# Performance work log

Hardware: AMD Instinct MI355X
Metric: run time of the kernel (lower is better)

## Reference

```python
import jax, jax.numpy as jnp
import numpy as np

DIST_THRESHOLD = 3.33  # threshold on SQUARED distances (pytorch3d knn_points.dists are squared)


def setup_inputs() -> dict:
    key = jax.random.key(0)
    k1, k2, k3, k4, k5, k6 = jax.random.split(key, 6)
    B, N, D = 4, 8192, 3
    points_src = jax.random.normal(k1, (B, N, D), dtype=jnp.float32)
    points_dst = jax.random.normal(k2, (B, N, D), dtype=jnp.float32)
    flows_pred = jax.random.normal(k3, (B, N, D), dtype=jnp.float32)
    flows_gt = jax.random.normal(k4, (B, N, D), dtype=jnp.float32)
    masks_src = jax.random.randint(k5, (B, N), 0, 2, dtype=jnp.int32)
    masks_dst = jax.random.randint(k6, (B, N), 0, 2, dtype=jnp.int32)
    return {"points_src": points_src, "points_dst": points_dst,
            "flows_pred": flows_pred, "flows_gt": flows_gt,
            "masks_src": masks_src, "masks_dst": masks_dst}


def _pairwise_sq_dists(a, b):
    # a: [N,3], b: [M,3] -> [N,M] squared euclidean distances via gram trick
    a2 = jnp.sum(a * a, axis=-1)  # [N]
    b2 = jnp.sum(b * b, axis=-1)  # [M]
    d2 = a2[:, None] + b2[None, :] - 2.0 * (a @ b.T)
    return jnp.maximum(d2, 0.0)


def _chamfer_thresholded(pw, pd, ms, md):
    # pw: warped src points [N,3]; pd: dst points [M,3]; ms/md: validity masks (>0)
    valid_s = ms > 0  # [N]
    valid_d = md > 0  # [M]
    d2 = _pairwise_sq_dists(pw, pd)  # [N,M]
    # K=1 NN in each direction; invalid points in the *search* set get +inf
    d_wt = jnp.min(jnp.where(valid_d[None, :], d2, jnp.inf), axis=1)  # [N]
    d_tw = jnp.min(jnp.where(valid_s[:, None], d2, jnp.inf), axis=0)  # [M]
    # thresholded mean over valid query points (mirrors boolean-index + .mean())
    sel_wt = valid_s & (d_wt < DIST_THRESHOLD)
    sel_tw = valid_d & (d_tw < DIST_THRESHOLD)
    mean_wt = jnp.sum(jnp.where(sel_wt, d_wt, 0.0)) / jnp.sum(sel_wt)
    mean_tw = jnp.sum(jnp.where(sel_tw, d_tw, 0.0)) / jnp.sum(sel_tw)
    return mean_wt + mean_tw


def reference(points_src, points_dst, flows_pred, flows_gt, masks_src, masks_dst):
    points_src_warped = points_src + flows_pred  # [B,N,3]
    per_sample = jax.vmap(_chamfer_thresholded)(points_src_warped, points_dst,
                                                masks_src, masks_dst)  # [B]
    return jnp.sum(per_sample)
```

## Files before the change

kernel.cpp:

```cpp
#include <hip/hip_runtime.h>
#include <hip/hip_bf16.h>

#define NPTS 8192
#define NB   4
#define BLK  256
#define NREG 32
#define QPT  4
#define NQC  (NREG / QPT)
#define NSL  16
#define SLICE_MAX 512
#define CAP  NPTS
#define THR  3.33f

#define OFF_PSUM 4096
#define OFF_PCNT 8192
#define OFF_BEST 16384
#define OFF_PTS  (16384 + 8 * CAP * 4)

__device__ __forceinline__ unsigned enc_f(float f) {
    unsigned u = __float_as_uint(f);
    return (u & 0x80000000u) ? ~u : (u | 0x80000000u);
}
__device__ __forceinline__ float dec_f(unsigned u) {
    return (u & 0x80000000u) ? __uint_as_float(u & 0x7FFFFFFFu)
                             : __uint_as_float(~u);
}

__global__ __launch_bounds__(BLK) void compact_kernel(
    const float* __restrict__ Ps, const float* __restrict__ Pd,
    const float* __restrict__ F,  const int* __restrict__ Ms,
    const int* __restrict__ Md,   unsigned* __restrict__ bcnt,
    float4* __restrict__ pts,     unsigned* __restrict__ best)
{
    const int b = blockIdx.z, side = blockIdx.y, r = blockIdx.x;
    const int qi = b * 2 + side;
    const int tid = threadIdx.x;
    const int g = b * NPTS + r * BLK + tid;

    best[(size_t)qi * CAP + r * BLK + tid] = 0u;

    float x, y, z; int v;
    if (side == 0) {
        x = Ps[3 * g + 0] + F[3 * g + 0];
        y = Ps[3 * g + 1] + F[3 * g + 1];
        z = Ps[3 * g + 2] + F[3 * g + 2];
        v = Ms[g];
    } else {
        x = Pd[3 * g + 0]; y = Pd[3 * g + 1]; z = Pd[3 * g + 2];
        v = Md[g];
    }
    const bool valid = v > 0;

    const int lane = tid & 63, w = tid >> 6;
    unsigned long long m = __ballot(valid);
    const int my = __popcll(m & ((1ull << lane) - 1ull));
    __shared__ int wc[4];
    if (lane == 0) wc[w] = __popcll(m);
    __syncthreads();
    int off = 0;
#pragma unroll
    for (int i = 0; i < 4; ++i) if (i < w) off += wc[i];
    if (valid)
        pts[(size_t)qi * CAP + r * BLK + off + my] =
            make_float4(2.f * x, 2.f * y, 2.f * z, -(x * x + y * y + z * z));
    if (tid == 0)
        bcnt[qi * NREG + r] = (unsigned)(wc[0] + wc[1] + wc[2] + wc[3]);
}

__global__ __launch_bounds__(BLK) void knn_kernel(
    const unsigned* __restrict__ bcnt, const float4* __restrict__ pts,
    unsigned* __restrict__ best)
{
    const int b = blockIdx.z, d = blockIdx.y;
    const int qc = blockIdx.x / NSL, sl = blockIdx.x % NSL;
    const int qi = b * 2 + d;
    const int si = b * 2 + (1 - d);
    const int tid = threadIdx.x;

    const int r0 = 2 * sl, r1 = 2 * sl + 1;
    const int c0 = (int)bcnt[si * NREG + r0];
    const int c1 = (int)bcnt[si * NREG + r1];
    const int len = c0 + c1;

    __shared__ float4 sp[SLICE_MAX];
    const float4* __restrict__ s0 = pts + (size_t)si * CAP + r0 * BLK;
    const float4* __restrict__ s1 = pts + (size_t)si * CAP + r1 * BLK;
    if (tid < c0) sp[tid] = s0[tid];
    if (tid < c1) sp[c0 + tid] = s1[tid];
    __syncthreads();

    float qx[QPT], qy[QPT], qz[QPT], bt[QPT];
    bool qv[QPT]; int qr[QPT];
#pragma unroll
    for (int k = 0; k < QPT; ++k) {
        qr[k] = qc * QPT + k;
        qv[k] = tid < (int)bcnt[qi * NREG + qr[k]];
        const float4 p = pts[(size_t)qi * CAP + qr[k] * BLK + tid];
        qx[k] = 0.5f * p.x; qy[k] = 0.5f * p.y; qz[k] = 0.5f * p.z;
        bt[k] = -1e30f;
    }

#pragma unroll 4
    for (int j = 0; j < len; ++j) {
        const float4 s = sp[j];
#pragma unroll
        for (int k = 0; k < QPT; ++k) {
            float t = fmaf(qx[k], s.x, s.w);
            t = fmaf(qy[k], s.y, t);
            t = fmaf(qz[k], s.z, t);
            bt[k] = fmaxf(bt[k], t);
        }
    }

#pragma unroll
    for (int k = 0; k < QPT; ++k)
        if (qv[k])
            atomicMax(&best[(size_t)qi * CAP + qr[k] * BLK + tid], enc_f(bt[k]));
}

__global__ __launch_bounds__(BLK) void finalize_kernel(
    const unsigned* __restrict__ bcnt, const float4* __restrict__ pts,
    const unsigned* __restrict__ best, float* __restrict__ psum,
    float* __restrict__ pcnt)
{
    const int b = blockIdx.z, side = blockIdx.y, r = blockIdx.x;
    const int qi = b * 2 + side;
    const int tid = threadIdx.x;
    float s = 0.f, c = 0.f;
    if (tid < (int)bcnt[qi * NREG + r]) {
        const float4 p = pts[(size_t)qi * CAP + r * BLK + tid];
        const float t = dec_f(best[(size_t)qi * CAP + r * BLK + tid]);
        float dd = fmaxf((-p.w) - t, 0.f);
        if (dd < THR) { s = dd; c = 1.f; }
    }
#pragma unroll
    for (int off = 32; off; off >>= 1) {
        s += __shfl_down(s, off);
        c += __shfl_down(c, off);
    }
    __shared__ float red[8];
    const int w = tid >> 6;
    if ((tid & 63) == 0) { red[w] = s; red[4 + w] = c; }
    __syncthreads();
    if (tid == 0) {
        psum[qi * NREG + r] = red[0] + red[1] + red[2] + red[3];
        pcnt[qi * NREG + r] = red[4] + red[5] + red[6] + red[7];
    }
}

__global__ void reduce_out_kernel(const float* __restrict__ psum,
                                  const float* __restrict__ pcnt,
                                  float* __restrict__ out)
{
    const int tid = threadIdx.x;
    float a = 0.f;
    if (tid < 8) {
        float s = 0.f, c = 0.f;
        for (int r = 0; r < NREG; ++r) {
            s += psum[tid * NREG + r];
            c += pcnt[tid * NREG + r];
        }
        a = s / c;
    }
#pragma unroll
    for (int off = 4; off; off >>= 1) a += __shfl_down(a, off);
    if (tid == 0) out[0] = a;
}

extern "C" void kernel_launch(void* const* d_in, const int* in_sizes, int n_in,
                              void* d_out, int out_size, void* d_ws, size_t ws_size,
                              hipStream_t stream)
{
    const float* Ps = (const float*)d_in[0];
    const float* Pd = (const float*)d_in[1];
    const float* F  = (const float*)d_in[2];
    const int* Ms = (const int*)d_in[4];
    const int* Md = (const int*)d_in[5];
    float* out = (float*)d_out;

    unsigned* bcnt = (unsigned*)d_ws;
    float* psum = (float*)((char*)d_ws + OFF_PSUM);
    float* pcnt = (float*)((char*)d_ws + OFF_PCNT);
    unsigned* best = (unsigned*)((char*)d_ws + OFF_BEST);
    float4* pts = (float4*)((char*)d_ws + OFF_PTS);

    compact_kernel<<<dim3(NREG, 2, NB), BLK, 0, stream>>>(
        Ps, Pd, F, Ms, Md, bcnt, pts, best);

    knn_kernel<<<dim3(NQC * NSL, 2, NB), BLK, 0, stream>>>(bcnt, pts, best);

    finalize_kernel<<<dim3(NREG, 2, NB), BLK, 0, stream>>>(
        bcnt, pts, best, psum, pcnt);

    reduce_out_kernel<<<1, 64, 0, stream>>>(psum, pcnt, out);
}
```

Measured before the change: 35.62 us.

## Densely pack valid points via prefix sums to skip empty query and search slots

Each kernel now builds prefix sums over the per-region valid counts and addresses the compacted points as one contiguous logical array, mapping each id to its region by binary search. Query chunks past the valid count exit early, and the search set is split into equal slices, which doubles the slice count. With roughly half of the points masked out, about half of the query blocks can skip their work and the loads are more evenly balanced. The cost is an extra scan and per-point binary search in shared memory, plus an extra sync.

```diff
diff --git a/kernel.cpp b/kernel.cpp
--- a/kernel.cpp
+++ b/kernel.cpp
@@ -6,9 +6,10 @@
 #define BLK  256
 #define NREG 32
 #define QPT  4
-#define NQC  (NREG / QPT)
-#define NSL  16
-#define SLICE_MAX 512
+#define QPB  (QPT * BLK)
+#define NQC_MAX (NPTS / QPB)
+#define NSL  32
+#define SMAX ((NPTS + NSL - 1) / NSL)
 #define CAP  NPTS
 #define THR  3.33f
 
@@ -24,6 +25,29 @@
 __device__ __forceinline__ float dec_f(unsigned u) {
     return (u & 0x80000000u) ? __uint_as_float(u & 0x7FFFFFFFu)
                              : __uint_as_float(~u);
+}
+
+__device__ __forceinline__ void build_prefix(const unsigned* __restrict__ bcnt,
+                                             int qi, int* P, int tid) {
+    if (tid < 64) {
+        const int lane = tid & 63;
+        int v = (lane < NREG) ? (int)bcnt[qi * NREG + lane] : 0;
+#pragma unroll
+        for (int o = 1; o < NREG; o <<= 1) {
+            int t = __shfl_up(v, o);
+            if (lane >= o) v += t;
+        }
+        if (lane < NREG) P[lane + 1] = v;
+        if (lane == 0) P[0] = 0;
+    }
+}
+
+__device__ __forceinline__ int map_region(const int* P, int id) {
+    int r = 0;
+#pragma unroll
+    for (int s = 16; s; s >>= 1)
+        if (P[r + s] <= id) r += s;
+    return r;
 }
 
 __global__ __launch_bounds__(BLK) void compact_kernel(
@@ -77,25 +101,47 @@
     const int si = b * 2 + (1 - d);
     const int tid = threadIdx.x;
 
-    const int r0 = 2 * sl, r1 = 2 * sl + 1;
-    const int c0 = (int)bcnt[si * NREG + r0];
-    const int c1 = (int)bcnt[si * NREG + r1];
-    const int len = c0 + c1;
-
-    __shared__ float4 sp[SLICE_MAX];
-    const float4* __restrict__ s0 = pts + (size_t)si * CAP + r0 * BLK;
-    const float4* __restrict__ s1 = pts + (size_t)si * CAP + r1 * BLK;
-    if (tid < c0) sp[tid] = s0[tid];
-    if (tid < c1) sp[c0 + tid] = s1[tid];
+    __shared__ int Pq[NREG + 1], Psx[NREG + 1];
+    __shared__ float4 sp[SMAX];
+
+    if (tid < 64) {
+        const int lane = tid & 63;
+        int vq = (lane < NREG) ? (int)bcnt[qi * NREG + lane] : 0;
+        int vs = (lane < NREG) ? (int)bcnt[si * NREG + lane] : 0;
+#pragma unroll
+        for (int o = 1; o < NREG; o <<= 1) {
+            int tq = __shfl_up(vq, o);
+            int ts = __shfl_up(vs, o);
+            if (lane >= o) { vq += tq; vs += ts; }
+        }
+        if (lane < NREG) { Pq[lane + 1] = vq; Psx[lane + 1] = vs; }
+        if (lane == 0) { Pq[0] = 0; Psx[0] = 0; }
+    }
+    __syncthreads();
+
+    const int nq = Pq[NREG], ns = Psx[NREG];
+    if (qc * QPB >= nq) return;
+    const int L = (ns + NSL - 1) / NSL;
+    const int start = sl * L;
+    int len = ns - start; if (len > L) len = L;
+    if (len <= 0) return;
+
+    if (tid < len) {
+        const int id = start + tid;
+        const int r = map_region(Psx, id);
+        sp[tid] = pts[(size_t)si * CAP + r * BLK + (id - Psx[r])];
+    }
     __syncthreads();
 
     float qx[QPT], qy[QPT], qz[QPT], bt[QPT];
-    bool qv[QPT]; int qr[QPT];
+    bool qv[QPT]; int qn[QPT];
 #pragma unroll
     for (int k = 0; k < QPT; ++k) {
-        qr[k] = qc * QPT + k;
-        qv[k] = tid < (int)bcnt[qi * NREG + qr[k]];
-        const float4 p = pts[(size_t)qi * CAP + qr[k] * BLK + tid];
+        const int q = qc * QPB + k * BLK + tid;
+        qn[k] = q; qv[k] = q < nq;
+        const int qq = qv[k] ? q : 0;
+        const int r = map_region(Pq, qq);
+        const float4 p = pts[(size_t)qi * CAP + r * BLK + (qq - Pq[r])];
         qx[k] = 0.5f * p.x; qy[k] = 0.5f * p.y; qz[k] = 0.5f * p.z;
         bt[k] = -1e30f;
     }
@@ -115,7 +161,7 @@
 #pragma unroll
     for (int k = 0; k < QPT; ++k)
         if (qv[k])
-            atomicMax(&best[(size_t)qi * CAP + qr[k] * BLK + tid], enc_f(bt[k]));
+            atomicMax(&best[(size_t)qi * CAP + qn[k]], enc_f(bt[k]));
 }
 
 __global__ __launch_bounds__(BLK) void finalize_kernel(
@@ -123,13 +169,21 @@
     const unsigned* __restrict__ best, float* __restrict__ psum,
     float* __restrict__ pcnt)
 {
-    const int b = blockIdx.z, side = blockIdx.y, r = blockIdx.x;
+    const int b = blockIdx.z, side = blockIdx.y, bx = blockIdx.x;
     const int qi = b * 2 + side;
     const int tid = threadIdx.x;
+
+    __shared__ int Pq[NREG + 1];
+    build_prefix(bcnt, qi, Pq, tid);
+    __syncthreads();
+
+    const int nq = Pq[NREG];
+    const int q = bx * BLK + tid;
     float s = 0.f, c = 0.f;
-    if (tid < (int)bcnt[qi * NREG + r]) {
-        const float4 p = pts[(size_t)qi * CAP + r * BLK + tid];
-        const float t = dec_f(best[(size_t)qi * CAP + r * BLK + tid]);
+    if (q < nq) {
+        const int r = map_region(Pq, q);
+        const float4 p = pts[(size_t)qi * CAP + r * BLK + (q - Pq[r])];
+        const float t = dec_f(best[(size_t)qi * CAP + q]);
         float dd = fmaxf((-p.w) - t, 0.f);
         if (dd < THR) { s = dd; c = 1.f; }
     }
@@ -143,8 +197,8 @@
     if ((tid & 63) == 0) { red[w] = s; red[4 + w] = c; }
     __syncthreads();
     if (tid == 0) {
-        psum[qi * NREG + r] = red[0] + red[1] + red[2] + red[3];
-        pcnt[qi * NREG + r] = red[4] + red[5] + red[6] + red[7];
+        psum[qi * NREG + bx] = red[0] + red[1] + red[2] + red[3];
+        pcnt[qi * NREG + bx] = red[4] + red[5] + red[6] + red[7];
     }
 }
 
@@ -187,7 +241,7 @@
     compact_kernel<<<dim3(NREG, 2, NB), BLK, 0, stream>>>(
         Ps, Pd, F, Ms, Md, bcnt, pts, best);
 
-    knn_kernel<<<dim3(NQC * NSL, 2, NB), BLK, 0, stream>>>(bcnt, pts, best);
+    knn_kernel<<<dim3(NQC_MAX * NSL, 2, NB), BLK, 0, stream>>>(bcnt, pts, best);
 
     finalize_kernel<<<dim3(NREG, 2, NB), BLK, 0, stream>>>(
         bcnt, pts, best, psum, pcnt);
```

Result: faster. 33.97 us (-4.6%).
